# Optimization experiments

Hardware: AMD Instinct MI355X
Metric: run time of the kernel (lower is better)

Reference implementation:

```python
import jax, jax.numpy as jnp
import numpy as np

H = 16      # headNum
C = 64      # cDim
D = 1024    # qDim = kDim = vDim = outDim
N = 2       # batch
S = 1024    # seq len


def setup_inputs() -> dict:
    key = jax.random.key(0)
    ks = jax.random.split(key, 12)
    inp = {
        "Qin": jax.random.normal(ks[0], (N, S, D), dtype=jnp.float32),
        "Kin": jax.random.normal(ks[1], (N, S, D), dtype=jnp.float32),
        "Vin": jax.random.normal(ks[2], (N, S, D), dtype=jnp.float32),
        "seqMask": jax.random.randint(ks[3], (N, S), 0, 2).astype(jnp.bool_),
        "attMask": jax.random.normal(ks[4], (1, 1, S, S), dtype=jnp.float32),
        # learned parameters (stored as [in, out] for x @ W)
        "QTrans": jax.random.normal(ks[5], (D, H * C), dtype=jnp.float32) * 0.02,
        "KTrans": jax.random.normal(ks[6], (D, H * C), dtype=jnp.float32) * 0.02,
        "VTrans": jax.random.normal(ks[7], (D, H * C), dtype=jnp.float32) * 0.02,
        "GTrans_w": jax.random.normal(ks[8], (D, H * C), dtype=jnp.float32) * 0.02,
        "GTrans_b": jnp.ones((H * C,), dtype=jnp.float32),
        "out_w": jax.random.normal(ks[9], (H * C, D), dtype=jnp.float32) * 0.02,
        "out_b": jnp.zeros((D,), dtype=jnp.float32),
    }
    return inp


def _split_heads(x):
    # [n, s, h*c] -> [h, n, s, c]
    n, s, _ = x.shape
    return x.reshape(n, s, H, C).transpose(2, 0, 1, 3)


def reference(Qin, Kin, Vin, seqMask, attMask, QTrans, KTrans, VTrans,
              GTrans_w, GTrans_b, out_w, out_b):
    Q = _split_heads(Qin @ QTrans)                         # [h,n,s,c]
    K = _split_heads(Kin @ KTrans)                         # [h,n,t,c]
    V = _split_heads(Vin @ VTrans)                         # [h,n,t,c]
    G = jax.nn.sigmoid(_split_heads(Vin @ GTrans_w + GTrans_b))  # [h,n,s,c]

    scale = 1.0 / jnp.sqrt(jnp.float32(C))
    A = jnp.einsum('hnsi,hnti->hnst', Q, K) * scale        # [h,n,s,t]
    # masked_fill where outer-product of seqMask is True
    m = (seqMask[:, :, None] & seqMask[:, None, :])[None]  # [1,n,s,t]
    A = jnp.where(m, -jnp.inf, A)
    A = A + attMask
    A = jax.nn.softmax(A, axis=-1)
    # gated attention-value reduction (eval mode: dropout inactive)
    O = jnp.einsum('hnst,hnti,hnsi->nshi', A, V, G)        # [n,s,h,c]
    O = O.reshape(O.shape[0], O.shape[1], -1)              # [n,s,h*c]
    return O @ out_w + out_b
```

## Files before the change

### kernel.cpp

```cpp
#include <hip/hip_runtime.h>
#include <hip/hip_bf16.h>
#include <cstddef>

#define S_   1024
#define HC_  1024
#define C_   64
#define LOG2E 1.4426950408889634f
#define SC2   0.18033688011112042f

typedef __attribute__((ext_vector_type(8))) short bf16x8;
typedef __attribute__((ext_vector_type(4))) short bf16x4;
typedef __attribute__((ext_vector_type(4))) float f32x4;

typedef __attribute__((address_space(1))) const void gconst_t;
typedef __attribute__((address_space(3))) void lds_t;

__device__ __forceinline__ short cvt_bf16(float f) {
  union { float f; unsigned u; } v; v.f = f;
  unsigned r = v.u + 0x7FFFu + ((v.u >> 16) & 1u);
  return (short)(r >> 16);
}
__device__ __forceinline__ float bf2f(short s) {
  union { float f; unsigned u; } v; v.u = ((unsigned)(unsigned short)s) << 16;
  return v.f;
}

__global__ __launch_bounds__(256) void prep(
    const float* __restrict__ QT, const float* __restrict__ KT,
    const float* __restrict__ VT, const float* __restrict__ GW,
    const float* __restrict__ OW, short* __restrict__ WTb,
    const float* __restrict__ Qin, const float* __restrict__ Kin,
    const float* __restrict__ Vin, short* __restrict__ Abf,
    const float* __restrict__ att, const unsigned char* __restrict__ sm,
    short* __restrict__ biasP) {
  __shared__ short tile[32][33];
  __shared__ int a1, a4;
  const int bid = blockIdx.x;
  const int t = threadIdx.x;

  if (bid < 5120) {
    const int which = bid >> 10, xb = bid & 1023;
    const float* src = (which == 0) ? QT : (which == 1) ? KT : (which == 2) ? VT
                      : (which == 3) ? GW : OW;
    short* dst = WTb + (size_t)which * (1024u * 1024u);
    const int tj = (xb & 31) * 32;
    const int tk = (xb >> 5) * 32;
    const int r = t >> 3, c4 = (t & 7) * 4;
    const float4 v = *(const float4*)(src + (size_t)(tk + r) * 1024 + tj + c4);
    tile[c4 + 0][r] = cvt_bf16(v.x);
    tile[c4 + 1][r] = cvt_bf16(v.y);
    tile[c4 + 2][r] = cvt_bf16(v.z);
    tile[c4 + 3][r] = cvt_bf16(v.w);
    __syncthreads();
    bf16x4 o;
    o[0] = tile[r][c4 + 0]; o[1] = tile[r][c4 + 1];
    o[2] = tile[r][c4 + 2]; o[3] = tile[r][c4 + 3];
    *(bf16x4*)(dst + (size_t)(tj + r) * 1024 + tk + c4) = o;
  } else if (bid < 8192) {
    const int idx = bid - 5120;
    const int y = idx >> 10, xb = idx & 1023;
    const float* src = (y == 0) ? Qin : (y == 1) ? Kin : Vin;
    short* d = Abf + (size_t)y * 2097152u;
    const int i = (xb * 256 + t) * 8;
    const float4 a = *(const float4*)(src + i);
    const float4 b = *(const float4*)(src + i + 4);
    bf16x8 o;
    o[0] = cvt_bf16(a.x); o[1] = cvt_bf16(a.y); o[2] = cvt_bf16(a.z); o[3] = cvt_bf16(a.w);
    o[4] = cvt_bf16(b.x); o[5] = cvt_bf16(b.y); o[6] = cvt_bf16(b.z); o[7] = cvt_bf16(b.w);
    *(bf16x8*)(d + i) = o;
  } else {
    if (t == 0) { a1 = 0; a4 = 0; }
    __syncthreads();
    int l1 = 0, l4 = 0;
    for (int i = t; i < 2048; i += 256) {
      if (sm[i]) { if (i & 3) l1 = 1; else if (i & 4) l4 = 1; }
    }
    if (l1) atomicOr(&a1, 1);
    if (l4) atomicOr(&a4, 1);
    __syncthreads();
    const int mst = a1 ? 1 : (a4 ? 4 : 8);

    const int idx = bid - 8192;
    const int qw = idx & 63, tt = (idx >> 6) & 15, n = idx >> 10;
    const int lslot = t >> 2, i4 = t & 3;
    const int tc = tt * 64 + i4 * 16 + (lslot & 15);
    const int qbase = qw * 16 + ((lslot >> 4) << 2);
    const int smt = sm[(size_t)(n * 1024 + tc) * mst];
    bf16x4 o;
#pragma unroll
    for (int ii = 0; ii < 4; ii++) {
      const int q = qbase + ii;
      const int smq = sm[(size_t)(n * 1024 + q) * mst];
      const float val = (smq && smt) ? -1e4f : att[(size_t)q * 1024 + tc] * LOG2E;
      o[ii] = cvt_bf16(val);
    }
    short* dst = biasP + (((size_t)(n * 64 + qw) * 16 + tt) * 64 + lslot) * 16 + i4 * 4;
    *(bf16x4*)dst = o;
  }
}

__global__ __launch_bounds__(256) void v_transpose(
    const short* __restrict__ Vp, short* __restrict__ VpT) {
  __shared__ short tile[32][33];
  const int n = blockIdx.y;
  const int tc = (blockIdx.x & 31) * 32;
  const int ts = (blockIdx.x >> 5) * 32;
  const int t = threadIdx.x;
  const int r = t >> 3, c4 = (t & 7) * 4;
  bf16x4 v = *(const bf16x4*)(Vp + (size_t)(n * S_ + ts + r) * HC_ + tc + c4);
  tile[c4 + 0][r] = v[0]; tile[c4 + 1][r] = v[1];
  tile[c4 + 2][r] = v[2]; tile[c4 + 3][r] = v[3];
  __syncthreads();
  bf16x4 o;
  o[0] = tile[r][c4 + 0]; o[1] = tile[r][c4 + 1];
  o[2] = tile[r][c4 + 2]; o[3] = tile[r][c4 + 3];
  *(bf16x4*)(VpT + ((size_t)n * HC_ + tc + r) * S_ + ts + c4) = o;
}

template<int MW, int NW>
__device__ __forceinline__ void gemm_core_bf(
    const short* __restrict__ A, const short* __restrict__ BT,
    short* As, short* Bs, int m0, int n0, f32x4 acc[MW][NW]) {
  const int t = threadIdx.x;
  const int lane = t & 63, wid = t >> 6;
  const int wr = wid >> 1, wc = wid & 1;
  const int l15 = lane & 15, g = lane >> 4;

#pragma unroll
  for (int m = 0; m < MW; m++)
#pragma unroll
    for (int n2 = 0; n2 < NW; n2++) acc[m][n2] = (f32x4){0.f, 0.f, 0.f, 0.f};

#define STAGE_(buf, kt)                                                        \
  {                                                                            \
    const int k0_ = (kt) * 32;                                                 \
    _Pragma("unroll")                                                          \
    for (int i_ = 0; i_ < NW / 2; i_++) {                                      \
      const int seg_ = i_ * 256 + t;                                           \
      const int row_ = seg_ >> 2, gl_ = seg_ & 3;                              \
      __builtin_amdgcn_global_load_lds(                                        \
          (gconst_t*)(BT + (size_t)(n0 + row_) * 1024 + k0_ +                  \
                      ((gl_ ^ ((row_ >> 1) & 3)) * 8)),                        \
          (lds_t*)(Bs + (buf) * (NW * 1024) + seg_ * 8), 16, 0, 0);            \
    }                                                                          \
    _Pragma("unroll")                                                          \
    for (int i_ = 0; i_ < MW / 2; i_++) {                                      \
      const int seg_ = i_ * 256 + t;                                           \
      const int row_ = seg_ >> 2, gl_ = seg_ & 3;                              \
      __builtin_amdgcn_global_load_lds(                                        \
          (gconst_t*)(A + (size_t)(m0 + row_) * 1024 + k0_ +                   \
                      ((gl_ ^ ((row_ >> 1) & 3)) * 8)),                        \
          (lds_t*)(As + (buf) * (MW * 1024) + seg_ * 8), 16, 0, 0);            \
    }                                                                          \
  }

  STAGE_(0, 0);
  __syncthreads();
  int cur = 0;
  for (int kt = 0; kt < 32; ++kt) {
    if (kt + 1 < 32) STAGE_(cur ^ 1, kt + 1);
    const short* Ac = As + cur * (MW * 1024);
    const short* Bc = Bs + cur * (NW * 1024);
    bf16x8 a[MW], b[NW];
#pragma unroll
    for (int m = 0; m < MW; m++) {
      const int row = wr * (MW * 16) + m * 16 + l15;
      a[m] = *(const bf16x8*)(Ac + row * 32 + ((g ^ ((row >> 1) & 3)) * 8));
    }
#pragma unroll
    for (int n2 = 0; n2 < NW; n2++) {
      const int row = wc * (NW * 16) + n2 * 16 + l15;
      b[n2] = *(const bf16x8*)(Bc + row * 32 + ((g ^ ((row >> 1) & 3)) * 8));
    }
    __builtin_amdgcn_s_setprio(1);
#pragma unroll
    for (int m = 0; m < MW; m++)
#pragma unroll
      for (int n2 = 0; n2 < NW; n2++)
        acc[m][n2] = __builtin_amdgcn_mfma_f32_16x16x32_bf16(a[m], b[n2], acc[m][n2], 0, 0, 0);
    __builtin_amdgcn_s_setprio(0);
    __syncthreads();
    cur ^= 1;
  }
#undef STAGE_
}

__global__ __launch_bounds__(256) void gemm_proj(
    const short* __restrict__ Abf, const short* __restrict__ WTb,
    short* __restrict__ Pb, const float* __restrict__ gb) {
  __shared__ short As[2 * 4096];
  __shared__ short Bs[2 * 2048];
  const int y = blockIdx.y;
  const short* A = Abf + (size_t)((y <= 2) ? y : 2) * 2097152u;
  const short* BT = WTb + (size_t)y * (1024u * 1024u);
  short* outp = Pb + (size_t)y * 2097152u;
  const int bid = blockIdx.x;
  const int m0 = (bid & 15) * 128, n0 = (bid >> 4) * 64;
  f32x4 acc[4][2];
  gemm_core_bf<4, 2>(A, BT, As, Bs, m0, n0, acc);
  const int t = threadIdx.x, lane = t & 63, wid = t >> 6;
  const int wr = wid >> 1, wc = wid & 1, l15 = lane & 15, g = lane >> 4;
#pragma unroll
  for (int m = 0; m < 4; m++)
#pragma unroll
    for (int n2 = 0; n2 < 2; n2++)
#pragma unroll
      for (int j = 0; j < 4; j++) {
        const int row = m0 + wr * 64 + m * 16 + g * 4 + j;
        const int col = n0 + wc * 32 + n2 * 16 + l15;
        float v = acc[m][n2][j];
        if (y == 3) { v += gb[col]; v = 1.0f / (1.0f + __expf(-v)); }
        outp[(size_t)row * 1024 + col] = cvt_bf16(v);
      }
}

__global__ __launch_bounds__(256) void gemm_final(
    const short* __restrict__ Aobuf, const short* __restrict__ WTo,
    float* __restrict__ outp, const float* __restrict__ ob) {
  __shared__ short As[2 * 2048];
  __shared__ short Bs[2 * 2048];
  const int bid = blockIdx.x;
  const int m0 = (bid & 31) * 64, n0 = (bid >> 5) * 64;
  f32x4 acc[2][2];
  gemm_core_bf<2, 2>(Aobuf, WTo, As, Bs, m0, n0, acc);
  const int t = threadIdx.x, lane = t & 63, wid = t >> 6;
  const int wr = wid >> 1, wc = wid & 1, l15 = lane & 15, g = lane >> 4;
#pragma unroll
  for (int m = 0; m < 2; m++)
#pragma unroll
    for (int n2 = 0; n2 < 2; n2++)
#pragma unroll
      for (int j = 0; j < 4; j++) {
        const int row = m0 + wr * 32 + m * 16 + g * 4 + j;
        const int col = n0 + wc * 32 + n2 * 16 + l15;
        outp[(size_t)row * 1024 + col] = acc[m][n2][j] + ob[col];
      }
}

__global__ __launch_bounds__(256) void attn_split(
    const short* __restrict__ Qp, const short* __restrict__ Kp,
    const short* __restrict__ VpT, const short* __restrict__ biasP,
    float* __restrict__ mlbuf, short* __restrict__ OpartB, int lns) {
  __shared__ short Ks[64 * 64];
  __shared__ short Vt[64 * 64];
  __shared__ short Pl[4][16 * 64];

  const int t = threadIdx.x;
  const int lane = t & 63, w = t >> 6;
  const int l15 = lane & 15, g = lane >> 4;
  const int xb = blockIdx.x, h = blockIdx.y, n = blockIdx.z;
  const int sp = xb & ((1 << lns) - 1), qb = xb >> lns;
  const int itc = 16 >> lns;

  const int sbase = qb * 64 + w * 16;
  const short* qptr = Qp + (size_t)(n * S_ + sbase + l15) * HC_ + h * C_;
  const bf16x8 qf0 = *(const bf16x8*)(qptr + g * 8);
  const bf16x8 qf1 = *(const bf16x8*)(qptr + 32 + g * 8);

  float mrow[4], lsum[4];
  f32x4 oacc[4];
#pragma unroll
  for (int j = 0; j < 4; j++) { mrow[j] = -1e30f; lsum[j] = 0.f; }
#pragma unroll
  for (int cb = 0; cb < 4; cb++) oacc[cb] = (f32x4){0.f, 0.f, 0.f, 0.f};

  const int str = t >> 3, sc8 = (t & 7) * 8;
  const short* bbase = biasP + ((size_t)(n * 64 + qb * 4 + w) * 16 * 64 + lane) * 16;

  {
    const int t0 = sp * itc * 64;
    bf16x8 kA0 = *(const bf16x8*)(Kp + (size_t)(n * S_ + t0 + str) * HC_ + h * C_ + sc8);
    bf16x8 kA1 = *(const bf16x8*)(Kp + (size_t)(n * S_ + t0 + 32 + str) * HC_ + h * C_ + sc8);
    bf16x8 vA0 = *(const bf16x8*)(VpT + ((size_t)n * HC_ + h * C_ + str) * S_ + t0 + sc8);
    bf16x8 vA1 = *(const bf16x8*)(VpT + ((size_t)n * HC_ + h * C_ + 32 + str) * S_ + t0 + sc8);

    for (int it = 0; it < itc; ++it) {
      const int tg = sp * itc + it;
      __syncthreads();
      { const int kr = str;      *(bf16x8*)((char*)Ks + kr * 128 + ((sc8 * 2) ^ ((kr & 7) << 4))) = kA0; }
      { const int kr = 32 + str; *(bf16x8*)((char*)Ks + kr * 128 + ((sc8 * 2) ^ ((kr & 7) << 4))) = kA1; }
      { const int cr = str;      *(bf16x8*)((char*)Vt + cr * 128 + ((sc8 * 2) ^ ((cr & 7) << 4))) = vA0; }
      { const int cr = 32 + str; *(bf16x8*)((char*)Vt + cr * 128 + ((sc8 * 2) ^ ((cr & 7) << 4))) = vA1; }
      __syncthreads();

      const bf16x8 bf0 = *(const bf16x8*)(bbase + tg * 1024);
      const bf16x8 bf1 = *(const bf16x8*)(bbase + tg * 1024 + 8);
      const int t1 = ((it + 1 < itc) ? (tg + 1) : tg) * 64;
      bf16x8 kB0 = *(const bf16x8*)(Kp + (size_t)(n * S_ + t1 + str) * HC_ + h * C_ + sc8);
      bf16x8 kB1 = *(const bf16x8*)(Kp + (size_t)(n * S_ + t1 + 32 + str) * HC_ + h * C_ + sc8);
      bf16x8 vB0 = *(const bf16x8*)(VpT + ((size_t)n * HC_ + h * C_ + str) * S_ + t1 + sc8);
      bf16x8 vB1 = *(const bf16x8*)(VpT + ((size_t)n * HC_ + h * C_ + 32 + str) * S_ + t1 + sc8);

      f32x4 sacc[4];
#pragma unroll
      for (int nb = 0; nb < 4; nb++) sacc[nb] = (f32x4){0.f, 0.f, 0.f, 0.f};
      __builtin_amdgcn_s_setprio(1);
#pragma unroll
      for (int nb = 0; nb < 4; nb++) {
        const int krow = nb * 16 + l15;
        const bf16x8 b0 = *(const bf16x8*)((char*)Ks + krow * 128 + ((g * 16) ^ ((krow & 7) << 4)));
        const bf16x8 b1 = *(const bf16x8*)((char*)Ks + krow * 128 + ((64 + g * 16) ^ ((krow & 7) << 4)));
        sacc[nb] = __builtin_amdgcn_mfma_f32_16x16x32_bf16(qf0, b0, sacc[nb], 0, 0, 0);
        sacc[nb] = __builtin_amdgcn_mfma_f32_16x16x32_bf16(qf1, b1, sacc[nb], 0, 0, 0);
      }
      __builtin_amdgcn_s_setprio(0);

      float tmax[4];
#pragma unroll
      for (int j = 0; j < 4; j++) tmax[j] = -1e30f;
#pragma unroll
      for (int nb = 0; nb < 4; nb++)
#pragma unroll
        for (int j = 0; j < 4; j++) {
          const short bb = (nb < 2) ? bf0[nb * 4 + j] : bf1[(nb - 2) * 4 + j];
          const float lg = sacc[nb][j] * SC2 + bf2f(bb);
          sacc[nb][j] = lg;
          tmax[j] = fmaxf(tmax[j], lg);
        }
#pragma unroll
      for (int j = 0; j < 4; j++) {
#pragma unroll
        for (int d = 1; d < 16; d <<= 1)
          tmax[j] = fmaxf(tmax[j], __shfl_xor(tmax[j], d, 64));
        const float mn = fmaxf(mrow[j], tmax[j]);
        const float sc = exp2f(mrow[j] - mn);
        mrow[j] = mn;
        lsum[j] *= sc;
#pragma unroll
        for (int cb = 0; cb < 4; cb++) oacc[cb][j] *= sc;
        float ps = 0.f;
#pragma unroll
        for (int nb = 0; nb < 4; nb++) {
          const float p = exp2f(sacc[nb][j] - mn);
          sacc[nb][j] = p;
          ps += p;
        }
        lsum[j] += ps;
      }
      short* Pw = &Pl[w][0];
#pragma unroll
      for (int nb = 0; nb < 4; nb++)
#pragma unroll
        for (int j = 0; j < 4; j++) {
          const int pr = g * 4 + j;
          const int pcb = (nb * 16 + l15) * 2;
          *(short*)((char*)Pw + pr * 128 + (pcb ^ ((pr & 7) << 4))) = cvt_bf16(sacc[nb][j]);
        }
      __builtin_amdgcn_s_setprio(1);
#pragma unroll
      for (int kk = 0; kk < 2; kk++) {
        const bf16x8 pf = *(const bf16x8*)((char*)Pw + l15 * 128 + ((kk * 64 + g * 16) ^ ((l15 & 7) << 4)));
#pragma unroll
        for (int cb = 0; cb < 4; cb++) {
          const int vrow = cb * 16 + l15;
          const bf16x8 vf = *(const bf16x8*)((char*)Vt + vrow * 128 + ((kk * 64 + g * 16) ^ ((vrow & 7) << 4)));
          oacc[cb] = __builtin_amdgcn_mfma_f32_16x16x32_bf16(pf, vf, oacc[cb], 0, 0, 0);
        }
      }
      __builtin_amdgcn_s_setprio(0);
      kA0 = kB0; kA1 = kB1; vA0 = vB0; vA1 = vB1;
    }
  }
  const int slot = (((n * 16 + h) * 16 + qb) << lns) + sp;
  short* op = OpartB + (size_t)slot * 4096;
  float* mlp = mlbuf + (size_t)slot * 128;
#pragma unroll
  for (int j = 0; j < 4; j++) {
    float rs = lsum[j];
#pragma unroll
    for (int d = 1; d < 16; d <<= 1) rs += __shfl_xor(rs, d, 64);
    const int row = w * 16 + g * 4 + j;
#pragma unroll
    for (int cb = 0; cb < 4; cb++)
      op[row * 64 + cb * 16 + l15] = cvt_bf16(oacc[cb][j]);
    if (l15 == 0) { mlp[row * 2] = mrow[j]; mlp[row * 2 + 1] = rs; }
  }
}

__global__ __launch_bounds__(256) void attn_merge(
    const short* __restrict__ OpartB, const float* __restrict__ mlbuf,
    const short* __restrict__ Gp, short* __restrict__ ObufB, int lns) {
  const int qb = blockIdx.x, h = blockIdx.y, n = blockIdx.z;
  const int nsplit = 1 << lns;
  const int t = threadIdx.x;
  const int r = t >> 2, c0 = (t & 3) * 16;
  const int bslot = ((n * 16 + h) * 16 + qb) << lns;
  const float* mlb = mlbuf + (size_t)bslot * 128 + r * 2;

  float M = -1e30f;
  for (int sp = 0; sp < nsplit; sp++) M = fmaxf(M, mlb[(size_t)sp * 128]);
  float l = 0.f;
  for (int sp = 0; sp < nsplit; sp++)
    l += exp2f(mlb[(size_t)sp * 128] - M) * mlb[(size_t)sp * 128 + 1];
  const float inv = 1.0f / l;

  float acc[16];
#pragma unroll
  for (int k = 0; k < 16; k++) acc[k] = 0.f;
  for (int sp = 0; sp < nsplit; sp++) {
    const float wsc = exp2f(mlb[(size_t)sp * 128] - M);
    const short* op = OpartB + (size_t)(bslot + sp) * 4096 + r * 64 + c0;
    const bf16x8 v0 = *(const bf16x8*)(op);
    const bf16x8 v1 = *(const bf16x8*)(op + 8);
#pragma unroll
    for (int k = 0; k < 8; k++) {
      acc[k]     += wsc * bf2f(v0[k]);
      acc[8 + k] += wsc * bf2f(v1[k]);
    }
  }
  const int srow = qb * 64 + r;
  const size_t idx = (size_t)(n * S_ + srow) * HC_ + h * C_ + c0;
  const bf16x8 g0 = *(const bf16x8*)(Gp + idx);
  const bf16x8 g1 = *(const bf16x8*)(Gp + idx + 8);
  bf16x8 o0, o1;
#pragma unroll
  for (int k = 0; k < 8; k++) {
    o0[k] = cvt_bf16(acc[k] * inv * bf2f(g0[k]));
    o1[k] = cvt_bf16(acc[8 + k] * inv * bf2f(g1[k]));
  }
  *(bf16x8*)(ObufB + idx) = o0;
  *(bf16x8*)(ObufB + idx + 8) = o1;
}

extern "C" void kernel_launch(void* const* d_in, const int* in_sizes, int n_in,
                              void* d_out, int out_size, void* d_ws, size_t ws_size,
                              hipStream_t stream) {
  const float* Qin      = (const float*)d_in[0];
  const float* Kin      = (const float*)d_in[1];
  const float* Vin      = (const float*)d_in[2];
  const void*  seqMask  = d_in[3];
  const float* attMask  = (const float*)d_in[4];
  const float* QTrans   = (const float*)d_in[5];
  const float* KTrans   = (const float*)d_in[6];
  const float* VTrans   = (const float*)d_in[7];
  const float* GTrans_w = (const float*)d_in[8];
  const float* GTrans_b = (const float*)d_in[9];
  const float* out_w    = (const float*)d_in[10];
  const float* out_b    = (const float*)d_in[11];
  float* out = (float*)d_out;

  char* ws = (char*)d_ws;
  const size_t MB = 1048576u;
  short* WTb   = (short*)(ws);
  short* Abf   = (short*)(ws + 10 * MB);
  short* Pb    = (short*)(ws + 22 * MB);
  short* VpT   = (short*)(ws + 38 * MB);
  short* ObufB = (short*)(ws + 42 * MB);
  short* biasP = (short*)(ws + 46 * MB);
  const size_t partBase = 51 * MB;

  const short* Kp = Pb + (size_t)1u * 2097152u;
  const short* Gp = Pb + (size_t)3u * 2097152u;

  int lns = 0;
  for (int c = 2; c >= 0; c--) {
    const size_t slots = 512u << c;
    if (ws_size >= partBase + slots * (8192u + 512u)) { lns = c; break; }
  }
  const size_t slots = 512u << lns;
  short* OpartB = (short*)(ws + partBase);
  float* mlbuf  = (float*)(ws + partBase + slots * 8192u);

  hipLaunchKernelGGL(prep, dim3(10240), dim3(256), 0, stream,
                     QTrans, KTrans, VTrans, GTrans_w, out_w, WTb,
                     Qin, Kin, Vin, Abf,
                     attMask, (const unsigned char*)seqMask, biasP);
  hipLaunchKernelGGL(gemm_proj, dim3(256, 4), dim3(256), 0, stream,
                     Abf, WTb, Pb, GTrans_b);
  hipLaunchKernelGGL(v_transpose, dim3(1024, 2), dim3(256), 0, stream,
                     Pb + (size_t)2u * 2097152u, VpT);
  hipLaunchKernelGGL(attn_split, dim3(16 << lns, 16, 2), dim3(256), 0, stream,
                     Pb, Kp, VpT, biasP, mlbuf, OpartB, lns);
  hipLaunchKernelGGL(attn_merge, dim3(16, 16, 2), dim3(256), 0, stream,
                     OpartB, mlbuf, Gp, ObufB, lns);
  hipLaunchKernelGGL(gemm_final, dim3(512), dim3(256), 0, stream,
                     ObufB, WTb + (size_t)4u * 1048576u, out, out_b);
}
```

Before: 112.4 us.

## Triple-buffer GEMM LDS staging with explicit vmcnt waits and barriers

Replaces the double-buffered global_load_lds pipeline in the shared GEMM core with a three-stage ring, prefetching two k-tiles ahead. Each iteration waits with explicit s_waitcnt vmcnt counts instead of a full __syncthreads drain, so in-flight loads for later tiles keep running across the barrier. This is meant to hide global memory latency behind the MFMA work, at the cost of more LDS per block, which may reduce occupancy.

```diff
diff --git a/kernel.cpp b/kernel.cpp
--- a/kernel.cpp
+++ b/kernel.cpp
@@ -23,6 +23,14 @@
 __device__ __forceinline__ float bf2f(short s) {
   union { float f; unsigned u; } v; v.u = ((unsigned)(unsigned short)s) << 16;
   return v.f;
+}
+
+template<int N> __device__ __forceinline__ void wait_vm() {
+  if constexpr (N == 0)      asm volatile("s_waitcnt vmcnt(0)" ::: "memory");
+  else if constexpr (N == 2) asm volatile("s_waitcnt vmcnt(2)" ::: "memory");
+  else if constexpr (N == 3) asm volatile("s_waitcnt vmcnt(3)" ::: "memory");
+  else if constexpr (N == 4) asm volatile("s_waitcnt vmcnt(4)" ::: "memory");
+  else if constexpr (N == 6) asm volatile("s_waitcnt vmcnt(6)" ::: "memory");
 }
 
 __global__ __launch_bounds__(256) void prep(
@@ -125,6 +133,10 @@
   const int lane = t & 63, wid = t >> 6;
   const int wr = wid >> 1, wc = wid & 1;
   const int l15 = lane & 15, g = lane >> 4;
+  constexpr int NT = 32;
+  constexpr int LDT = MW / 2 + NW / 2;
+  constexpr int ABUF = MW * 1024;
+  constexpr int BBUF = NW * 1024;
 
 #pragma unroll
   for (int m = 0; m < MW; m++)
@@ -141,7 +153,7 @@
       __builtin_amdgcn_global_load_lds(                                        \
           (gconst_t*)(BT + (size_t)(n0 + row_) * 1024 + k0_ +                  \
                       ((gl_ ^ ((row_ >> 1) & 3)) * 8)),                        \
-          (lds_t*)(Bs + (buf) * (NW * 1024) + seg_ * 8), 16, 0, 0);            \
+          (lds_t*)(Bs + (buf) * BBUF + seg_ * 8), 16, 0, 0);                   \
     }                                                                          \
     _Pragma("unroll")                                                          \
     for (int i_ = 0; i_ < MW / 2; i_++) {                                      \
@@ -150,17 +162,28 @@
       __builtin_amdgcn_global_load_lds(                                        \
           (gconst_t*)(A + (size_t)(m0 + row_) * 1024 + k0_ +                   \
                       ((gl_ ^ ((row_ >> 1) & 3)) * 8)),                        \
-          (lds_t*)(As + (buf) * (MW * 1024) + seg_ * 8), 16, 0, 0);            \
+          (lds_t*)(As + (buf) * ABUF + seg_ * 8), 16, 0, 0);                   \
     }                                                                          \
   }
 
   STAGE_(0, 0);
-  __syncthreads();
-  int cur = 0;
-  for (int kt = 0; kt < 32; ++kt) {
-    if (kt + 1 < 32) STAGE_(cur ^ 1, kt + 1);
-    const short* Ac = As + cur * (MW * 1024);
-    const short* Bc = Bs + cur * (NW * 1024);
+  STAGE_(1, 1);
+  int b0 = 0, b1 = 1, b2 = 2;
+  for (int kt = 0; kt < NT; ++kt) {
+    if (kt + 2 < NT) {
+      STAGE_(b2, kt + 2);
+      wait_vm<2 * LDT>();
+    } else if (kt + 2 == NT) {
+      wait_vm<LDT>();
+    } else {
+      wait_vm<0>();
+    }
+    __builtin_amdgcn_sched_barrier(0);
+    __builtin_amdgcn_s_barrier();
+    __builtin_amdgcn_sched_barrier(0);
+
+    const short* Ac = As + b0 * ABUF;
+    const short* Bc = Bs + b0 * BBUF;
     bf16x8 a[MW], b[NW];
 #pragma unroll
     for (int m = 0; m < MW; m++) {
@@ -179,8 +202,10 @@
       for (int n2 = 0; n2 < NW; n2++)
         acc[m][n2] = __builtin_amdgcn_mfma_f32_16x16x32_bf16(a[m], b[n2], acc[m][n2], 0, 0, 0);
     __builtin_amdgcn_s_setprio(0);
-    __syncthreads();
-    cur ^= 1;
+    __builtin_amdgcn_sched_barrier(0);
+    __builtin_amdgcn_s_barrier();
+    __builtin_amdgcn_sched_barrier(0);
+    const int tmp = b0; b0 = b1; b1 = b2; b2 = tmp;
   }
 #undef STAGE_
 }
@@ -188,8 +213,8 @@
 __global__ __launch_bounds__(256) void gemm_proj(
     const short* __restrict__ Abf, const short* __restrict__ WTb,
     short* __restrict__ Pb, const float* __restrict__ gb) {
-  __shared__ short As[2 * 4096];
-  __shared__ short Bs[2 * 2048];
+  __shared__ short As[3 * 4096];
+  __shared__ short Bs[3 * 2048];
   const int y = blockIdx.y;
   const short* A = Abf + (size_t)((y <= 2) ? y : 2) * 2097152u;
   const short* BT = WTb + (size_t)y * (1024u * 1024u);
@@ -217,8 +242,8 @@
 __global__ __launch_bounds__(256) void gemm_final(
     const short* __restrict__ Aobuf, const short* __restrict__ WTo,
     float* __restrict__ outp, const float* __restrict__ ob) {
-  __shared__ short As[2 * 2048];
-  __shared__ short Bs[2 * 2048];
+  __shared__ short As[3 * 2048];
+  __shared__ short Bs[3 * 2048];
   const int bid = blockIdx.x;
   const int m0 = (bid & 31) * 64, n0 = (bid >> 5) * 64;
   f32x4 acc[2][2];
```

New measurement: 119.4 us. 6.2% more time.
